# Performance work log

Hardware: AMD Instinct MI355X
Metric: run time of the kernel (lower is better)

Reference implementation:

```python
import jax, jax.numpy as jnp
import numpy as np

E, T, D_IN, D_H = 8, 4096, 2048, 1408

def setup_inputs() -> dict:
    key = jax.random.key(0)
    k_x, k_g, k_d, k_u = jax.random.split(key, 4)
    x = jax.random.normal(k_x, (E, T, D_IN), dtype=jnp.float32)
    gate_proj = jax.random.normal(k_g, (E, D_IN, D_H), dtype=jnp.float32) * 0.02
    down_proj = jax.random.normal(k_d, (E, D_IN, D_H), dtype=jnp.float32) * 0.02
    up_proj = jax.random.normal(k_u, (E, D_H, D_IN), dtype=jnp.float32) * 0.02
    return {"x": x, "gate_proj": gate_proj, "down_proj": down_proj,
            "up_proj": up_proj, "tokens_per_expert": T}

def reference(x, gate_proj, down_proj, up_proj, tokens_per_expert):
    # ep_size == 1 -> dispatch/combine are identity; x: [E, T, dim_in]
    # SwiGLU: h = silu(x @ gate) * (x @ down); out = h @ up
    h = jax.nn.silu(jnp.einsum('etd,edh->eth', x, gate_proj)) \
        * jnp.einsum('etd,edh->eth', x, down_proj)
    out = jnp.einsum('eth,ehd->etd', h, up_proj)
    return out
```

## Files before the change

kernel.cpp:

```cpp
#include <hip/hip_runtime.h>
#include <hip/hip_bf16.h>


typedef __bf16 bf16x8 __attribute__((ext_vector_type(8)));
typedef float  f32x4  __attribute__((ext_vector_type(4)));

__device__ __forceinline__ void gload16(const void* g, void* l) {
  __builtin_amdgcn_global_load_lds((const __attribute__((address_space(1))) void*)g,
                                   (__attribute__((address_space(3))) void*)l,
                                   16, 0, 0);
}

__device__ __forceinline__ unsigned short f2bf(float f) {
  union { float fv; unsigned u; } v; v.fv = f;
  unsigned r = (v.u + 0x7fffu + ((v.u >> 16) & 1u)) >> 16;
  return (unsigned short)r;
}

__global__ __launch_bounds__(256)
void cvt_f32_bf16(const float* __restrict__ in, unsigned short* __restrict__ out,
                  long n) {
  long i = ((long)blockIdx.x * 256 + threadIdx.x) * 4;
  const long stride = (long)gridDim.x * 1024;
  for (; i < n; i += stride) {
    const float4 v = *(const float4*)(in + i);
    ushort4 o;
    o.x = f2bf(v.x); o.y = f2bf(v.y); o.z = f2bf(v.z); o.w = f2bf(v.w);
    *(ushort4*)(out + i) = o;
  }
}

__global__ __launch_bounds__(256)
void trcvt(const float* __restrict__ in, unsigned short* __restrict__ out,
           int R, int C) {
  __shared__ unsigned short tile[32][33];
  const float* src = in + (size_t)blockIdx.z * R * C;
  unsigned short* dst = out + (size_t)blockIdx.z * R * C;
  const int c0 = blockIdx.x << 5, r0 = blockIdx.y << 5;
  const int tx = threadIdx.x, ty = threadIdx.y;
#pragma unroll
  for (int i = 0; i < 32; i += 8)
    tile[ty + i][tx] = f2bf(src[(size_t)(r0 + ty + i) * C + (c0 + tx)]);
  __syncthreads();
#pragma unroll
  for (int i = 0; i < 32; i += 8)
    dst[(size_t)(c0 + ty + i) * R + (r0 + tx)] = tile[tx][ty + i];
}

template <int KDIM, int NDIM, bool FUSED, bool F32OUT>
__global__ __launch_bounds__(512, 2)
void gemm8p(const unsigned short* __restrict__ A,
            const unsigned short* __restrict__ B0,
            const unsigned short* __restrict__ B1,
            void* __restrict__ Cout) {
  constexpr int BM  = 256;
  constexpr int BN  = FUSED ? 128 : 256;
  constexpr int NB_N = NDIM / BN;
  constexpr int NKT = KDIM / 64;
  constexpr int PMI = FUSED ? 2 : 4;
  constexpr int NMI = FUSED ? 4 : 8;

  __shared__ __align__(16) unsigned short sA[2][BM * 64];
  __shared__ __align__(16) unsigned short sB[2][(FUSED ? 2 : 1) * BN * 64];

  const int t = threadIdx.x;
  const int w = t >> 6;
  const int lane = t & 63;
  const int e = blockIdx.y;

  const int cpx = gridDim.x >> 3;
  const int bid = (blockIdx.x & 7) * cpx + (blockIdx.x >> 3);
  const int m0 = (bid / NB_N) << 8;
  const int n0 = (bid % NB_N) * BN;

  const unsigned short* Ae  = A  + (size_t)e * 4096 * KDIM;
  const unsigned short* B0e = B0 + (size_t)e * NDIM * KDIM;

  const int l8 = lane >> 3;
  const int lc = ((lane & 7) ^ l8) << 3;

  const unsigned short* aSrc[4];
  const unsigned short* bSrc[4];
#pragma unroll
  for (int i = 0; i < 4; ++i)
    aSrc[i] = Ae + (size_t)(m0 + ((4 * w + i) << 3) + l8) * KDIM + lc;
  if constexpr (FUSED) {
    const unsigned short* B1e = B1 + (size_t)e * NDIM * KDIM;
#pragma unroll
    for (int j = 0; j < 2; ++j) {
      bSrc[j]     = B0e + (size_t)(n0 + ((2 * w + j) << 3) + l8) * KDIM + lc;
      bSrc[2 + j] = B1e + (size_t)(n0 + ((2 * w + j) << 3) + l8) * KDIM + lc;
    }
  } else {
#pragma unroll
    for (int i = 0; i < 4; ++i)
      bSrc[i] = B0e + (size_t)(n0 + ((4 * w + i) << 3) + l8) * KDIM + lc;
  }

  auto stage = [&](int nb) {
#pragma unroll
    for (int i = 0; i < 4; ++i) {
      gload16(aSrc[i], &sA[nb][(4 * w + i) << 9]);
      aSrc[i] += 64;
    }
    if constexpr (FUSED) {
#pragma unroll
      for (int j = 0; j < 2; ++j) {
        gload16(bSrc[j], &sB[nb][(2 * w + j) << 9]);
        bSrc[j] += 64;
        gload16(bSrc[2 + j], &sB[nb][(BN * 64) + ((2 * w + j) << 9)]);
        bSrc[2 + j] += 64;
      }
    } else {
#pragma unroll
      for (int i = 0; i < 4; ++i) {
        gload16(bSrc[i], &sB[nb][(4 * w + i) << 9]);
        bSrc[i] += 64;
      }
    }
  };

  const int wm = FUSED ? ((w >> 1) << 6) : ((w >> 2) << 7);
  const int wn = FUSED ? ((w & 1) << 6) : ((w & 3) << 6);
  const int lm = lane & 15;
  const int kq = lane >> 4;

  f32x4 acc0[NMI][4];
  f32x4 acc1[FUSED ? 4 : 1][4];
  const f32x4 z = {0.f, 0.f, 0.f, 0.f};
#pragma unroll
  for (int mi = 0; mi < NMI; ++mi)
#pragma unroll
    for (int ni = 0; ni < 4; ++ni) acc0[mi][ni] = z;
  if constexpr (FUSED) {
#pragma unroll
    for (int mi = 0; mi < 4; ++mi)
#pragma unroll
      for (int ni = 0; ni < 4; ++ni) acc1[mi][ni] = z;
  }

  bf16x8 af[PMI][2], bf0[2][2], bf1[2][2];

  auto ldf = [&](const unsigned short* base, int rowbase, int ks) -> bf16x8 {
    const int r = rowbase + lm;
    const int c = ((ks << 2) + kq) ^ (lm & 7);
    return ((const bf16x8*)base)[(r << 3) + c];
  };

#define PHASE(bufA, bufB, ABLK, BPAIR, READA, TILEEND)                         \
  {                                                                            \
    if constexpr (READA) {                                                     \
      _Pragma("unroll") for (int mi = 0; mi < PMI; ++mi)                       \
        _Pragma("unroll") for (int ks = 0; ks < 2; ++ks)                       \
          af[mi][ks] = ldf(bufA, wm + (((ABLK)*PMI + mi) << 4), ks);           \
    }                                                                          \
    _Pragma("unroll") for (int nj = 0; nj < 2; ++nj)                           \
      _Pragma("unroll") for (int ks = 0; ks < 2; ++ks) {                       \
        bf0[nj][ks] = ldf(bufB, wn + (((BPAIR)*2 + nj) << 4), ks);             \
        if constexpr (FUSED)                                                   \
          bf1[nj][ks] = ldf((bufB) + BN * 64, wn + (((BPAIR)*2 + nj) << 4), ks); \
      }                                                                        \
    __builtin_amdgcn_s_barrier();                                              \
    asm volatile("s_waitcnt lgkmcnt(0)" ::: "memory");                         \
    __builtin_amdgcn_s_setprio(1);                                             \
    _Pragma("unroll") for (int mi = 0; mi < PMI; ++mi)                         \
      _Pragma("unroll") for (int nj = 0; nj < 2; ++nj)                         \
        _Pragma("unroll") for (int ks = 0; ks < 2; ++ks) {                     \
          acc0[(ABLK)*PMI + mi][(BPAIR)*2 + nj] =                              \
              __builtin_amdgcn_mfma_f32_16x16x32_bf16(                         \
                  af[mi][ks], bf0[nj][ks],                                     \
                  acc0[(ABLK)*PMI + mi][(BPAIR)*2 + nj], 0, 0, 0);             \
          if constexpr (FUSED)                                                 \
            acc1[(ABLK)*PMI + mi][(BPAIR)*2 + nj] =                            \
                __builtin_amdgcn_mfma_f32_16x16x32_bf16(                       \
                    af[mi][ks], bf1[nj][ks],                                   \
                    acc1[(ABLK)*PMI + mi][(BPAIR)*2 + nj], 0, 0, 0);           \
        }                                                                      \
    __builtin_amdgcn_s_setprio(0);                                             \
    if constexpr (TILEEND) asm volatile("s_waitcnt vmcnt(0)" ::: "memory");    \
    __builtin_amdgcn_s_barrier();                                              \
  }

  stage(0);
  asm volatile("s_waitcnt vmcnt(0)" ::: "memory");
  __builtin_amdgcn_s_barrier();

  for (int kt = 0; kt < NKT; ++kt) {
    const int cur = kt & 1;
    const unsigned short* bufA = sA[cur];
    const unsigned short* bufB = sB[cur];
    if (kt + 1 < NKT) stage(cur ^ 1);
    PHASE(bufA, bufB, 0, 0, true,  false)
    PHASE(bufA, bufB, 0, 1, false, false)
    PHASE(bufA, bufB, 1, 0, true,  false)
    PHASE(bufA, bufB, 1, 1, false, true)
  }
#undef PHASE

  const size_t cbase = (size_t)e * 4096 * NDIM;
  if constexpr (F32OUT) {
    float* C = (float*)Cout + cbase;
#pragma unroll
    for (int mi = 0; mi < NMI; ++mi)
#pragma unroll
      for (int ni = 0; ni < 4; ++ni)
#pragma unroll
        for (int i = 0; i < 4; ++i) {
          const int row = m0 + wm + (mi << 4) + (kq << 2) + i;
          const int col = n0 + wn + (ni << 4) + lm;
          C[(size_t)row * NDIM + col] = acc0[mi][ni][i];
        }
  } else {
    unsigned short* C = (unsigned short*)Cout + cbase;
#pragma unroll
    for (int mi = 0; mi < NMI; ++mi)
#pragma unroll
      for (int ni = 0; ni < 4; ++ni)
#pragma unroll
        for (int i = 0; i < 4; ++i) {
          const int row = m0 + wm + (mi << 4) + (kq << 2) + i;
          const int col = n0 + wn + (ni << 4) + lm;
          const float g = acc0[mi][ni][i];
          const float d = acc1[mi][ni][i];
          C[(size_t)row * NDIM + col] = f2bf(g / (1.0f + __expf(-g)) * d);
        }
  }
}

extern "C" void kernel_launch(void* const* d_in, const int* in_sizes, int n_in,
                              void* d_out, int out_size, void* d_ws, size_t ws_size,
                              hipStream_t stream) {
  const float* x    = (const float*)d_in[0];
  const float* gate = (const float*)d_in[1];
  const float* down = (const float*)d_in[2];
  const float* up   = (const float*)d_in[3];

  unsigned short* xb = (unsigned short*)d_out;

  char* ws = (char*)d_ws;
  unsigned short* h    = (unsigned short*)ws;
  unsigned short* bufG = (unsigned short*)(ws + 92274688ull);
  unsigned short* bufD = (unsigned short*)(ws + 138412032ull);

  const long nx = 8L * 4096 * 2048;
  cvt_f32_bf16<<<8192, 256, 0, stream>>>(x, xb, nx);

  dim3 tb(32, 8, 1);
  trcvt<<<dim3(44, 64, 8), tb, 0, stream>>>(gate, bufG, 2048, 1408);
  trcvt<<<dim3(44, 64, 8), tb, 0, stream>>>(down, bufD, 2048, 1408);

  gemm8p<2048, 1408, true, false><<<dim3(176, 8), 512, 0, stream>>>(xb, bufG, bufD, h);

  trcvt<<<dim3(64, 44, 8), tb, 0, stream>>>(up, bufG, 1408, 2048);

  gemm8p<1408, 2048, false, true><<<dim3(128, 8), 512, 0, stream>>>(h, bufG, nullptr, (float*)d_out);
}
```

Before: 1.459 ms.

## Replace double-buffered K=64 GEMM pipeline with 4-slot K=32 LDS ring

Both GEMM kernels now use a four-slot shared-memory ring with K=32 steps in place of two K=64 buffers. Loads run three stages ahead and are split into A and B halves that are issued between the two MFMA phases. The LDS swizzle and fragment indexing change to match the new 32-wide rows. The aim is deeper global-to-LDS prefetch, so memory latency hides better behind compute. The cost is twice as many K iterations, each with barriers, and finer-grained vmcnt bookkeeping that must stay correct.

```diff
diff --git a/kernel.cpp b/kernel.cpp
--- a/kernel.cpp
+++ b/kernel.cpp
@@ -49,19 +49,16 @@
 
 template <int KDIM, int NDIM, bool FUSED, bool F32OUT>
 __global__ __launch_bounds__(512, 2)
-void gemm8p(const unsigned short* __restrict__ A,
-            const unsigned short* __restrict__ B0,
-            const unsigned short* __restrict__ B1,
-            void* __restrict__ Cout) {
-  constexpr int BM  = 256;
-  constexpr int BN  = FUSED ? 128 : 256;
+void gemm_ring(const unsigned short* __restrict__ A,
+               const unsigned short* __restrict__ B0,
+               const unsigned short* __restrict__ B1,
+               void* __restrict__ Cout) {
+  constexpr int BN   = FUSED ? 128 : 256;
   constexpr int NB_N = NDIM / BN;
-  constexpr int NKT = KDIM / 64;
-  constexpr int PMI = FUSED ? 2 : 4;
-  constexpr int NMI = FUSED ? 4 : 8;
-
-  __shared__ __align__(16) unsigned short sA[2][BM * 64];
-  __shared__ __align__(16) unsigned short sB[2][(FUSED ? 2 : 1) * BN * 64];
+  constexpr int NS   = KDIM / 32;
+  constexpr int SLOT = 16384;
+
+  __shared__ __align__(16) unsigned short lds[4 * SLOT];
 
   const int t = threadIdx.x;
   const int w = t >> 6;
@@ -74,128 +71,126 @@
   const int n0 = (bid % NB_N) * BN;
 
   const unsigned short* Ae  = A  + (size_t)e * 4096 * KDIM;
-  const unsigned short* B0e = B0 + (size_t)e * NDIM * KDIM;
-
-  const int l8 = lane >> 3;
-  const int lc = ((lane & 7) ^ l8) << 3;
-
-  const unsigned short* aSrc[4];
-  const unsigned short* bSrc[4];
-#pragma unroll
-  for (int i = 0; i < 4; ++i)
-    aSrc[i] = Ae + (size_t)(m0 + ((4 * w + i) << 3) + l8) * KDIM + lc;
+  const unsigned short* Be0 = B0 + (size_t)e * NDIM * KDIM;
+
+  const int prow = lane >> 2;
+  const int pcol = (((lane & 3) ^ ((lane >> 3) & 3)) << 3);
+
+  const unsigned short* s0 = Ae + (size_t)(m0 + (w << 4) + prow) * KDIM + pcol;
+  const unsigned short* s1 = Ae + (size_t)(m0 + ((w + 8) << 4) + prow) * KDIM + pcol;
+  const unsigned short* s2;
+  const unsigned short* s3;
   if constexpr (FUSED) {
-    const unsigned short* B1e = B1 + (size_t)e * NDIM * KDIM;
-#pragma unroll
-    for (int j = 0; j < 2; ++j) {
-      bSrc[j]     = B0e + (size_t)(n0 + ((2 * w + j) << 3) + l8) * KDIM + lc;
-      bSrc[2 + j] = B1e + (size_t)(n0 + ((2 * w + j) << 3) + l8) * KDIM + lc;
-    }
+    const unsigned short* Be1 = B1 + (size_t)e * NDIM * KDIM;
+    s2 = Be0 + (size_t)(n0 + (w << 4) + prow) * KDIM + pcol;
+    s3 = Be1 + (size_t)(n0 + (w << 4) + prow) * KDIM + pcol;
   } else {
-#pragma unroll
-    for (int i = 0; i < 4; ++i)
-      bSrc[i] = B0e + (size_t)(n0 + ((4 * w + i) << 3) + l8) * KDIM + lc;
-  }
-
-  auto stage = [&](int nb) {
-#pragma unroll
-    for (int i = 0; i < 4; ++i) {
-      gload16(aSrc[i], &sA[nb][(4 * w + i) << 9]);
-      aSrc[i] += 64;
-    }
-    if constexpr (FUSED) {
-#pragma unroll
-      for (int j = 0; j < 2; ++j) {
-        gload16(bSrc[j], &sB[nb][(2 * w + j) << 9]);
-        bSrc[j] += 64;
-        gload16(bSrc[2 + j], &sB[nb][(BN * 64) + ((2 * w + j) << 9)]);
-        bSrc[2 + j] += 64;
-      }
-    } else {
-#pragma unroll
-      for (int i = 0; i < 4; ++i) {
-        gload16(bSrc[i], &sB[nb][(4 * w + i) << 9]);
-        bSrc[i] += 64;
-      }
-    }
+    s2 = Be0 + (size_t)(n0 + (w << 4) + prow) * KDIM + pcol;
+    s3 = Be0 + (size_t)(n0 + ((w + 8) << 4) + prow) * KDIM + pcol;
+  }
+  const int d0 = (w << 9);
+  const int d1 = ((w + 8) << 9);
+  const int d2 = 8192 + (w << 9);
+  const int d3 = FUSED ? (12288 + (w << 9))
+                       : (8192 + ((w + 8) << 9));
+
+  auto stageA = [&](int slot) {
+    unsigned short* b = &lds[slot * SLOT];
+    gload16(s0, b + d0); s0 += 32;
+    gload16(s1, b + d1); s1 += 32;
+  };
+  auto stageB = [&](int slot) {
+    unsigned short* b = &lds[slot * SLOT];
+    gload16(s2, b + d2); s2 += 32;
+    gload16(s3, b + d3); s3 += 32;
   };
 
   const int wm = FUSED ? ((w >> 1) << 6) : ((w >> 2) << 7);
   const int wn = FUSED ? ((w & 1) << 6) : ((w & 3) << 6);
+  const int apan = wm >> 4;
+  const int bpan = wn >> 4;
   const int lm = lane & 15;
   const int kq = lane >> 4;
-
+  const int fo = lm * 4 + (kq ^ ((lm >> 1) & 3));
+
+  constexpr int NMI = FUSED ? 4 : 8;
   f32x4 acc0[NMI][4];
   f32x4 acc1[FUSED ? 4 : 1][4];
   const f32x4 z = {0.f, 0.f, 0.f, 0.f};
 #pragma unroll
   for (int mi = 0; mi < NMI; ++mi)
 #pragma unroll
-    for (int ni = 0; ni < 4; ++ni) acc0[mi][ni] = z;
+    for (int nj = 0; nj < 4; ++nj) acc0[mi][nj] = z;
   if constexpr (FUSED) {
 #pragma unroll
     for (int mi = 0; mi < 4; ++mi)
 #pragma unroll
-      for (int ni = 0; ni < 4; ++ni) acc1[mi][ni] = z;
-  }
-
-  bf16x8 af[PMI][2], bf0[2][2], bf1[2][2];
-
-  auto ldf = [&](const unsigned short* base, int rowbase, int ks) -> bf16x8 {
-    const int r = rowbase + lm;
-    const int c = ((ks << 2) + kq) ^ (lm & 7);
-    return ((const bf16x8*)base)[(r << 3) + c];
-  };
-
-#define PHASE(bufA, bufB, ABLK, BPAIR, READA, TILEEND)                         \
-  {                                                                            \
-    if constexpr (READA) {                                                     \
-      _Pragma("unroll") for (int mi = 0; mi < PMI; ++mi)                       \
-        _Pragma("unroll") for (int ks = 0; ks < 2; ++ks)                       \
-          af[mi][ks] = ldf(bufA, wm + (((ABLK)*PMI + mi) << 4), ks);           \
-    }                                                                          \
-    _Pragma("unroll") for (int nj = 0; nj < 2; ++nj)                           \
-      _Pragma("unroll") for (int ks = 0; ks < 2; ++ks) {                       \
-        bf0[nj][ks] = ldf(bufB, wn + (((BPAIR)*2 + nj) << 4), ks);             \
-        if constexpr (FUSED)                                                   \
-          bf1[nj][ks] = ldf((bufB) + BN * 64, wn + (((BPAIR)*2 + nj) << 4), ks); \
-      }                                                                        \
-    __builtin_amdgcn_s_barrier();                                              \
-    asm volatile("s_waitcnt lgkmcnt(0)" ::: "memory");                         \
-    __builtin_amdgcn_s_setprio(1);                                             \
-    _Pragma("unroll") for (int mi = 0; mi < PMI; ++mi)                         \
-      _Pragma("unroll") for (int nj = 0; nj < 2; ++nj)                         \
-        _Pragma("unroll") for (int ks = 0; ks < 2; ++ks) {                     \
-          acc0[(ABLK)*PMI + mi][(BPAIR)*2 + nj] =                              \
-              __builtin_amdgcn_mfma_f32_16x16x32_bf16(                         \
-                  af[mi][ks], bf0[nj][ks],                                     \
-                  acc0[(ABLK)*PMI + mi][(BPAIR)*2 + nj], 0, 0, 0);             \
-          if constexpr (FUSED)                                                 \
-            acc1[(ABLK)*PMI + mi][(BPAIR)*2 + nj] =                            \
-                __builtin_amdgcn_mfma_f32_16x16x32_bf16(                       \
-                    af[mi][ks], bf1[nj][ks],                                   \
-                    acc1[(ABLK)*PMI + mi][(BPAIR)*2 + nj], 0, 0, 0);           \
-        }                                                                      \
-    __builtin_amdgcn_s_setprio(0);                                             \
-    if constexpr (TILEEND) asm volatile("s_waitcnt vmcnt(0)" ::: "memory");    \
-    __builtin_amdgcn_s_barrier();                                              \
-  }
-
-  stage(0);
-  asm volatile("s_waitcnt vmcnt(0)" ::: "memory");
+      for (int nj = 0; nj < 4; ++nj) acc1[mi][nj] = z;
+  }
+
+  bf16x8 af[4], bf0[4], bf1[4];
+
+  stageA(0); stageB(0);
+  stageA(1); stageB(1);
+  stageA(2); stageB(2);
+  asm volatile("s_waitcnt vmcnt(8)" ::: "memory");
   __builtin_amdgcn_s_barrier();
 
-  for (int kt = 0; kt < NKT; ++kt) {
-    const int cur = kt & 1;
-    const unsigned short* bufA = sA[cur];
-    const unsigned short* bufB = sB[cur];
-    if (kt + 1 < NKT) stage(cur ^ 1);
-    PHASE(bufA, bufB, 0, 0, true,  false)
-    PHASE(bufA, bufB, 0, 1, false, false)
-    PHASE(bufA, bufB, 1, 0, true,  false)
-    PHASE(bufA, bufB, 1, 1, false, true)
-  }
-#undef PHASE
+  for (int s = 0; s < NS; ++s) {
+    const unsigned short* buf = &lds[(s & 3) * SLOT];
+    const bf16x8* pA   = (const bf16x8*)buf;
+    const bf16x8* pB   = (const bf16x8*)(buf + 8192);
+    const bf16x8* pB1v = (const bf16x8*)(buf + 12288);
+    const bool pf = (s + 3 < NS);
+    const int ps = (s + 3) & 3;
+
+#pragma unroll
+    for (int mi = 0; mi < 4; ++mi) af[mi] = pA[(apan + mi) * 64 + fo];
+#pragma unroll
+    for (int nj = 0; nj < 4; ++nj) bf0[nj] = pB[(bpan + nj) * 64 + fo];
+    if (pf) stageA(ps);
+    __builtin_amdgcn_s_barrier();
+    __builtin_amdgcn_s_setprio(1);
+#pragma unroll
+    for (int mi = 0; mi < 4; ++mi)
+#pragma unroll
+      for (int nj = 0; nj < 4; ++nj)
+        acc0[mi][nj] = __builtin_amdgcn_mfma_f32_16x16x32_bf16(
+            af[mi], bf0[nj], acc0[mi][nj], 0, 0, 0);
+    __builtin_amdgcn_s_setprio(0);
+    __builtin_amdgcn_s_barrier();
+
+    if constexpr (FUSED) {
+#pragma unroll
+      for (int nj = 0; nj < 4; ++nj) bf1[nj] = pB1v[(bpan + nj) * 64 + fo];
+    } else {
+#pragma unroll
+      for (int mi = 0; mi < 4; ++mi) af[mi] = pA[(apan + 4 + mi) * 64 + fo];
+    }
+    if (pf) stageB(ps);
+    __builtin_amdgcn_s_barrier();
+    __builtin_amdgcn_s_setprio(1);
+    if constexpr (FUSED) {
+#pragma unroll
+      for (int mi = 0; mi < 4; ++mi)
+#pragma unroll
+        for (int nj = 0; nj < 4; ++nj)
+          acc1[mi][nj] = __builtin_amdgcn_mfma_f32_16x16x32_bf16(
+              af[mi], bf1[nj], acc1[mi][nj], 0, 0, 0);
+    } else {
+#pragma unroll
+      for (int mi = 0; mi < 4; ++mi)
+#pragma unroll
+        for (int nj = 0; nj < 4; ++nj)
+          acc0[4 + mi][nj] = __builtin_amdgcn_mfma_f32_16x16x32_bf16(
+              af[mi], bf0[nj], acc0[4 + mi][nj], 0, 0, 0);
+    }
+    __builtin_amdgcn_s_setprio(0);
+    if (s + 3 < NS)      asm volatile("s_waitcnt vmcnt(8)" ::: "memory");
+    else if (s + 2 < NS) asm volatile("s_waitcnt vmcnt(4)" ::: "memory");
+    else if (s + 1 < NS) asm volatile("s_waitcnt vmcnt(0)" ::: "memory");
+    __builtin_amdgcn_s_barrier();
+  }
 
   const size_t cbase = (size_t)e * 4096 * NDIM;
   if constexpr (F32OUT) {
@@ -203,25 +198,25 @@
 #pragma unroll
     for (int mi = 0; mi < NMI; ++mi)
 #pragma unroll
-      for (int ni = 0; ni < 4; ++ni)
+      for (int nj = 0; nj < 4; ++nj)
 #pragma unroll
         for (int i = 0; i < 4; ++i) {
           const int row = m0 + wm + (mi << 4) + (kq << 2) + i;
-          const int col = n0 + wn + (ni << 4) + lm;
-          C[(size_t)row * NDIM + col] = acc0[mi][ni][i];
+          const int col = n0 + wn + (nj << 4) + lm;
+          C[(size_t)row * NDIM + col] = acc0[mi][nj][i];
         }
   } else {
     unsigned short* C = (unsigned short*)Cout + cbase;
 #pragma unroll
-    for (int mi = 0; mi < NMI; ++mi)
-#pragma unroll
-      for (int ni = 0; ni < 4; ++ni)
+    for (int mi = 0; mi < 4; ++mi)
+#pragma unroll
+      for (int nj = 0; nj < 4; ++nj)
 #pragma unroll
         for (int i = 0; i < 4; ++i) {
           const int row = m0 + wm + (mi << 4) + (kq << 2) + i;
-          const int col = n0 + wn + (ni << 4) + lm;
-          const float g = acc0[mi][ni][i];
-          const float d = acc1[mi][ni][i];
+          const int col = n0 + wn + (nj << 4) + lm;
+          const float g = acc0[mi][nj][i];
+          const float d = acc1[mi][nj][i];
           C[(size_t)row * NDIM + col] = f2bf(g / (1.0f + __expf(-g)) * d);
         }
   }
@@ -249,9 +244,9 @@
   trcvt<<<dim3(44, 64, 8), tb, 0, stream>>>(gate, bufG, 2048, 1408);
   trcvt<<<dim3(44, 64, 8), tb, 0, stream>>>(down, bufD, 2048, 1408);
 
-  gemm8p<2048, 1408, true, false><<<dim3(176, 8), 512, 0, stream>>>(xb, bufG, bufD, h);
+  gemm_ring<2048, 1408, true, false><<<dim3(176, 8), 512, 0, stream>>>(xb, bufG, bufD, h);
 
   trcvt<<<dim3(64, 44, 8), tb, 0, stream>>>(up, bufG, 1408, 2048);
 
-  gemm8p<1408, 2048, false, true><<<dim3(128, 8), 512, 0, stream>>>(h, bufG, nullptr, (float*)d_out);
-}
+  gemm_ring<1408, 2048, false, true><<<dim3(128, 8), 512, 0, stream>>>(h, bufG, nullptr, (float*)d_out);
+}
```

Result: faster. 1.184 ms (-18.8%).
